# Kernel optimization log

Hardware: AMD Instinct MI355X
Metric: run time of the kernel (lower is better)

The kernel has to match this reference:

```python
import jax, jax.numpy as jnp
import numpy as np

D_MODEL = 1024
NUM_HEADS = 16
D_K = D_MODEL // NUM_HEADS
B, S = 2, 2048


def setup_inputs() -> dict:
    key = jax.random.key(0)
    ks = jax.random.split(key, 11)
    sc = 1.0 / np.sqrt(D_MODEL)
    return {
        "Q_input": jax.random.normal(ks[0], (B, S, D_MODEL), jnp.float32),
        "K_input": jax.random.normal(ks[1], (B, S, D_MODEL), jnp.float32),
        "V_input": jax.random.normal(ks[2], (B, S, D_MODEL), jnp.float32),
        "Wq": jax.random.normal(ks[3], (D_MODEL, D_MODEL), jnp.float32) * sc,
        "bq": jax.random.normal(ks[4], (D_MODEL,), jnp.float32) * 0.01,
        "Wk": jax.random.normal(ks[5], (D_MODEL, D_MODEL), jnp.float32) * sc,
        "bk": jax.random.normal(ks[6], (D_MODEL,), jnp.float32) * 0.01,
        "Wv": jax.random.normal(ks[7], (D_MODEL, D_MODEL), jnp.float32) * sc,
        "bv": jax.random.normal(ks[8], (D_MODEL,), jnp.float32) * 0.01,
        "Wo": jax.random.normal(ks[9], (D_MODEL, D_MODEL), jnp.float32) * sc,
        "bo": jax.random.normal(ks[10], (D_MODEL,), jnp.float32) * 0.01,
    }


def reference(Q_input, K_input, V_input, Wq, bq, Wk, bk, Wv, bv, Wo, bo):
    # Linear projections (torch Linear: x @ W.T + b)
    Q = Q_input @ Wq.T + bq  # [B,S,D]
    K = K_input @ Wk.T + bk
    V = V_input @ Wv.T + bv
    # split heads -> [B,H,S,dk]
    def split(x):
        return x.reshape(B, S, NUM_HEADS, D_K).transpose(0, 2, 1, 3)
    Qh, Kh, Vh = split(Q), split(K), split(V)
    scale = 1.0 / jnp.sqrt(jnp.asarray(D_K, Qh.dtype))
    scores = jnp.einsum('bhqd,bhkd->bhqk', Qh, Kh) * scale  # [B,H,S,S]
    attn = jax.nn.softmax(scores, axis=-1)
    ctx = jnp.einsum('bhqk,bhkd->bhqd', attn, Vh)  # [B,H,S,dk]
    concat = ctx.transpose(0, 2, 1, 3).reshape(B, S, D_MODEL)
    out = concat @ Wo.T + bo  # dropout is identity in eval
    return out
```

## Files before the change

kernel.cpp:

```cpp
#include <hip/hip_runtime.h>
#include <stdint.h>

#define DM   1024
#define NH   16
#define DKH  64
#define BBATCH 2
#define SEQ  2048
#define MTOK (BBATCH*SEQ)

typedef unsigned short u16;
typedef unsigned int   u32;
typedef __attribute__((ext_vector_type(8))) short  bf16x8;
typedef __attribute__((ext_vector_type(4))) float  f32x4;

struct PtrArr11 { const void* p[11]; };
struct U16Arr11 { u16* p[11]; };

__device__ __forceinline__ float bf2f(u16 u) {
  union { unsigned int i; float f; } z; z.i = ((unsigned int)u) << 16; return z.f;
}
__device__ __forceinline__ u16 f2bf(float f) {
  union { float f; unsigned int i; } z; z.f = f;
  unsigned int i = z.i + 0x7fffu + ((z.i >> 16) & 1u);
  return (u16)(i >> 16);
}

__device__ __forceinline__ bf16x8 u4_to_bf(u32 a, u32 b, u32 c, u32 d) {
  union { u32 u[4]; bf16x8 v; } z; z.u[0] = a; z.u[1] = b; z.u[2] = c; z.u[3] = d; return z.v;
}

__device__ __forceinline__ void gld16(const void* g, void* l) {
  __builtin_amdgcn_global_load_lds(
      (const __attribute__((address_space(1))) void*)g,
      (__attribute__((address_space(3))) void*)l,
      16, 0, 0);
}

__global__ void k_detect(const unsigned int* __restrict__ w, int* __restrict__ flag) {
  const int ln = threadIdx.x & 63;
  const unsigned int word = w[ln];
  const unsigned int ex = (word >> 7) & 0xFFu;
  const int hit = (ex >= 100u && ex <= 126u) ? 1 : 0;
  unsigned long long m = __ballot(hit);
  if (ln == 0) *flag = (__popcll(m) >= 40) ? 0 : 1;
}

__global__ __launch_bounds__(256) void k_convert_all(PtrArr11 src, U16Arr11 dst,
                                                     const int* __restrict__ flag) {
  if (*flag == 0) return;
  const int b = blockIdx.x;
  int seg, base;
  if      (b <  2048) { seg = 0;  base = 0;    }
  else if (b <  4096) { seg = 1;  base = 2048; }
  else if (b <  6144) { seg = 2;  base = 4096; }
  else if (b <  6656) { seg = 3;  base = 6144; }
  else if (b == 6656) { seg = 4;  base = 6656; }
  else if (b <  7169) { seg = 5;  base = 6657; }
  else if (b == 7169) { seg = 6;  base = 7169; }
  else if (b <  7682) { seg = 7;  base = 7170; }
  else if (b == 7682) { seg = 8;  base = 7682; }
  else if (b <  8195) { seg = 9;  base = 7683; }
  else                { seg = 10; base = 8195; }
  const int n = (seg < 3) ? (MTOK * DM) : ((seg & 1) ? (DM * DM) : DM);
  const int i0 = (b - base) * 2048 + threadIdx.x * 8;
  if (i0 >= n) return;
  const float* s = (const float*)src.p[seg] + i0;
  bf16x8 o;
#pragma unroll
  for (int j = 0; j < 8; ++j) o[j] = (short)f2bf(s[j]);
  *(bf16x8*)(dst.p[seg] + i0) = o;
}

__device__ __forceinline__ void gemm_body(const u16* __restrict__ X,
                                          const u16* __restrict__ W,
                                          const u16* __restrict__ bias,
                                          void* __restrict__ out,
                                          int isf32out)
{
  __shared__ __attribute__((aligned(16))) u16 sA[128 * 32];
  __shared__ __attribute__((aligned(16))) u16 sB[128 * 32];
  const int tid = threadIdx.x;
  const int ln = tid & 63, wv = tid >> 6;
  const int wm = wv & 1, wn = wv >> 1;
  const int m0 = blockIdx.y * 128, n0 = blockIdx.x * 128;
  const int fr = ln & 15, fq = ln >> 4;
  const int srow = ln >> 2, sslot = (ln & 3) * 8;

  f32x4 acc[4][4];
#pragma unroll
  for (int i = 0; i < 4; ++i)
#pragma unroll
    for (int j = 0; j < 4; ++j) acc[i][j] = (f32x4){0.f, 0.f, 0.f, 0.f};

  const u16* pA = X + (size_t)(m0 + wv * 32 + srow) * DM + sslot;
  const u16* pB = W + (size_t)(n0 + wv * 32 + srow) * DM + sslot;
  u16* lA0 = sA + (wv * 2) * 512; u16* lA1 = sA + (wv * 2 + 1) * 512;
  u16* lB0 = sB + (wv * 2) * 512; u16* lB1 = sB + (wv * 2 + 1) * 512;

  for (int k0 = 0; k0 < DM; k0 += 32) {
    gld16(pA + k0,            lA0);
    gld16(pA + 16 * DM + k0,  lA1);
    gld16(pB + k0,            lB0);
    gld16(pB + 16 * DM + k0,  lB1);
    asm volatile("s_waitcnt vmcnt(0)" ::: "memory");
    __syncthreads();

    bf16x8 af[4], bfg[4];
#pragma unroll
    for (int t = 0; t < 4; ++t) {
      af[t]  = *(const bf16x8*)(sA + (wm * 64 + t * 16 + fr) * 32 + fq * 8);
      bfg[t] = *(const bf16x8*)(sB + (wn * 64 + t * 16 + fr) * 32 + fq * 8);
    }
#pragma unroll
    for (int i = 0; i < 4; ++i)
#pragma unroll
      for (int j = 0; j < 4; ++j)
        acc[i][j] = __builtin_amdgcn_mfma_f32_16x16x32_bf16(af[i], bfg[j], acc[i][j], 0, 0, 0);
    __syncthreads();
  }

#pragma unroll
  for (int i = 0; i < 4; ++i) {
    const int row = m0 + wm * 64 + i * 16 + fq * 4;
#pragma unroll
    for (int j = 0; j < 4; ++j) {
      const int col = n0 + wn * 64 + j * 16 + fr;
      const float bv = bf2f(bias[col]);
#pragma unroll
      for (int r = 0; r < 4; ++r) {
        const float val = acc[i][j][r] + bv;
        const size_t idx = (size_t)(row + r) * DM + col;
        if (isf32out) ((float*)out)[idx] = val;
        else          ((u16*)out)[idx]   = f2bf(val);
      }
    }
  }
}

__device__ __forceinline__ void gemm_body_n64(const u16* __restrict__ X,
                                              const u16* __restrict__ W,
                                              const u16* __restrict__ bias,
                                              void* __restrict__ out,
                                              int isf32out)
{
  __shared__ __attribute__((aligned(16))) u16 sA[128 * 32];
  __shared__ __attribute__((aligned(16))) u16 sB[64 * 32];
  const int tid = threadIdx.x;
  const int ln = tid & 63, wv = tid >> 6;
  const int wm = wv >> 1, wn = wv & 1;
  const int m0 = blockIdx.y * 128, n0 = blockIdx.x * 64;
  const int fr = ln & 15, fq = ln >> 4;
  const int srow = ln >> 2, sslot = (ln & 3) * 8;

  f32x4 acc[4][2];
#pragma unroll
  for (int i = 0; i < 4; ++i)
#pragma unroll
    for (int j = 0; j < 2; ++j) acc[i][j] = (f32x4){0.f, 0.f, 0.f, 0.f};

  const u16* pA = X + (size_t)(m0 + wv * 32 + srow) * DM + sslot;
  const u16* pB = W + (size_t)(n0 + wv * 16 + srow) * DM + sslot;
  u16* lA0 = sA + (wv * 2) * 512; u16* lA1 = sA + (wv * 2 + 1) * 512;
  u16* lB  = sB + wv * 512;

  for (int k0 = 0; k0 < DM; k0 += 32) {
    gld16(pA + k0,           lA0);
    gld16(pA + 16 * DM + k0, lA1);
    gld16(pB + k0,           lB);
    asm volatile("s_waitcnt vmcnt(0)" ::: "memory");
    __syncthreads();

    bf16x8 af[4], bfg[2];
#pragma unroll
    for (int t = 0; t < 4; ++t)
      af[t]  = *(const bf16x8*)(sA + (wm * 64 + t * 16 + fr) * 32 + fq * 8);
#pragma unroll
    for (int t = 0; t < 2; ++t)
      bfg[t] = *(const bf16x8*)(sB + (wn * 32 + t * 16 + fr) * 32 + fq * 8);
#pragma unroll
    for (int i = 0; i < 4; ++i)
#pragma unroll
      for (int j = 0; j < 2; ++j)
        acc[i][j] = __builtin_amdgcn_mfma_f32_16x16x32_bf16(af[i], bfg[j], acc[i][j], 0, 0, 0);
    __syncthreads();
  }

#pragma unroll
  for (int i = 0; i < 4; ++i) {
    const int row = m0 + wm * 64 + i * 16 + fq * 4;
#pragma unroll
    for (int j = 0; j < 2; ++j) {
      const int col = n0 + wn * 32 + j * 16 + fr;
      const float bv = bf2f(bias[col]);
#pragma unroll
      for (int r = 0; r < 4; ++r) {
        const float val = acc[i][j][r] + bv;
        const size_t idx = (size_t)(row + r) * DM + col;
        if (isf32out) ((float*)out)[idx] = val;
        else          ((u16*)out)[idx]   = f2bf(val);
      }
    }
  }
}

__global__ __launch_bounds__(256, 2) void k_gemm_qkv(
    PtrArr11 orig, U16Arr11 conv, const int* __restrict__ flag,
    u16* oq, u16* ok, u16* ov)
{
  const int f = *flag;
  const int z = blockIdx.z;
  const u16* X  = f ? conv.p[z]         : (const u16*)orig.p[z];
  const u16* W  = f ? conv.p[3 + 2 * z] : (const u16*)orig.p[3 + 2 * z];
  const u16* bi = f ? conv.p[4 + 2 * z] : (const u16*)orig.p[4 + 2 * z];
  u16* o = (z == 0) ? oq : (z == 1) ? ok : ov;
  gemm_body(X, W, bi, o, 0);
}

__global__ __launch_bounds__(256, 2) void k_gemm_one(
    const u16* X, const void* Wo_o, const u16* Wo_c,
    const void* bo_o, const u16* bo_c, const int* __restrict__ flag, void* o)
{
  const int f = *flag;
  const u16* W  = f ? Wo_c : (const u16*)Wo_o;
  const u16* bi = f ? bo_c : (const u16*)bo_o;
  gemm_body_n64(X, W, bi, o, f);
}

__global__ __launch_bounds__(256) void k_transpose(const u16* __restrict__ in,
                                                   u16* __restrict__ out)
{
  __shared__ u16 t[64][66];
  const int b = blockIdx.z;
  const int s0 = blockIdx.x * 64, d0 = blockIdx.y * 64;
  const int c = threadIdx.x & 63, r0 = threadIdx.x >> 6;
#pragma unroll
  for (int i = 0; i < 16; ++i) {
    const int r = r0 + 4 * i;
    t[r][c] = in[(size_t)(b * SEQ + s0 + r) * DM + d0 + c];
  }
  __syncthreads();
#pragma unroll
  for (int i = 0; i < 16; ++i) {
    const int r = r0 + 4 * i;
    out[(size_t)(b * DM + d0 + r) * SEQ + s0 + c] = t[c][r];
  }
}

__global__ __launch_bounds__(256, 2) void k_attn(
    const u16* __restrict__ Qp, const u16* __restrict__ Kp,
    const u16* __restrict__ Vt, u16* __restrict__ ctx)
{
  __shared__ __attribute__((aligned(16))) u16 sK[2][64 * 64];

  const int tid = threadIdx.x;
  const int ln = tid & 63, wv = tid >> 6;
  const int bh = blockIdx.y;
  const int b = bh >> 4, h = bh & 15;
  const int q0 = blockIdx.x * 128 + wv * 32;
  const int fr = ln & 15, fq = ln >> 4;
  const int fr7 = fr & 7;

  const int srow = ln >> 3;
  const int scol = ((ln & 7) ^ srow) * 8;
  const u16* gK0 = Kp + (size_t)(b * SEQ + wv * 16 + srow) * DM + h * DKH + scol;
  u16* sKb = &sK[0][0];

  const u16* gVb = Vt + (size_t)(b * DM + h * DKH) * SEQ;

  bf16x8 qf[2][2];
#pragma unroll
  for (int qt = 0; qt < 2; ++qt)
#pragma unroll
    for (int ks = 0; ks < 2; ++ks) {
      const u16* src = Qp + (size_t)(b * SEQ + q0 + qt * 16 + fr) * DM + h * DKH + ks * 32 + fq * 8;
      bf16x8 v = *(const bf16x8*)src;
      bf16x8 w;
#pragma unroll
      for (int j = 0; j < 8; ++j) w[j] = (short)f2bf(bf2f((u16)v[j]) * 0.125f);
      qf[qt][ks] = w;
    }

  float l_a[2] = {0.f, 0.f};
  float l_b[2] = {0.f, 0.f};
  f32x4 o_acc[2][4];
#pragma unroll
  for (int qt = 0; qt < 2; ++qt)
#pragma unroll
    for (int dt = 0; dt < 4; ++dt) o_acc[qt][dt] = (f32x4){0.f, 0.f, 0.f, 0.f};

#define STAGE_K(pp, key0)                                      \
  do {                                                         \
    u16* kd = sKb + (pp) * 4096 + wv * 1024;                   \
    gld16(gK0 + (size_t)(key0) * DM, kd);                      \
    gld16(gK0 + (size_t)((key0) + 8) * DM, kd + 512);          \
  } while (0)

  STAGE_K(0, 0);
  asm volatile("s_waitcnt vmcnt(0)" ::: "memory");
  __syncthreads();

  int p = 0;
  for (int kb = 0; kb < SEQ / 64; ++kb) {
    const int key0 = kb * 64;

    bf16x8 vf[4][2];
#pragma unroll
    for (int dt = 0; dt < 4; ++dt)
#pragma unroll
      for (int ks = 0; ks < 2; ++ks)
        vf[dt][ks] = *(const bf16x8*)(gVb + (size_t)(dt * 16 + fr) * SEQ + key0 + ks * 32 + fq * 8);

    if (kb + 1 < SEQ / 64) STAGE_K(p ^ 1, key0 + 64);

    const u16* K = sKb + p * 4096;

    bf16x8 kf[4][2];
#pragma unroll
    for (int nt = 0; nt < 4; ++nt)
#pragma unroll
      for (int ks = 0; ks < 2; ++ks)
        kf[nt][ks] = *(const bf16x8*)(K + (nt * 16 + fr) * 64 + ((ks * 4 + fq) ^ fr7) * 8);

    u32 pw[2][2][4];
#pragma unroll
    for (int qt = 0; qt < 2; ++qt) {
      f32x4 s_acc[4];
#pragma unroll
      for (int nt = 0; nt < 4; ++nt) s_acc[nt] = (f32x4){0.f, 0.f, 0.f, 0.f};
      __builtin_amdgcn_s_setprio(1);
#pragma unroll
      for (int nt = 0; nt < 4; ++nt)
#pragma unroll
        for (int ks = 0; ks < 2; ++ks)
          s_acc[nt] = __builtin_amdgcn_mfma_f32_16x16x32_bf16(kf[nt][ks], qf[qt][ks], s_acc[nt], 0, 0, 0);
      __builtin_amdgcn_s_setprio(0);

      u32 w[4][2];
#pragma unroll
      for (int nt = 0; nt < 4; ++nt)
#pragma unroll
        for (int t = 0; t < 2; ++t) {
          const float e0 = __expf(s_acc[nt][2 * t]);
          const float e1 = __expf(s_acc[nt][2 * t + 1]);
          l_a[qt] += e0;
          l_b[qt] += e1;
          u32 wd;
          asm("v_cvt_pk_bf16_f32 %0, %1, %2" : "=v"(wd) : "v"(e0), "v"(e1));
          w[nt][t] = wd;
        }
#pragma unroll
      for (int ks = 0; ks < 2; ++ks) {
        u32 a0 = w[2 * ks][0], b0 = w[2 * ks + 1][0];
        u32 a1 = w[2 * ks][1], b1 = w[2 * ks + 1][1];
        asm("v_permlane32_swap_b32 %0, %1" : "+v"(a0), "+v"(b0));
        asm("v_permlane16_swap_b32 %0, %1" : "+v"(a0), "+v"(b0));
        asm("v_permlane32_swap_b32 %0, %1" : "+v"(a1), "+v"(b1));
        asm("v_permlane16_swap_b32 %0, %1" : "+v"(a1), "+v"(b1));
        pw[qt][ks][0] = a0; pw[qt][ks][1] = a1; pw[qt][ks][2] = b0; pw[qt][ks][3] = b1;
      }
    }

#pragma unroll
    for (int dt = 0; dt < 4; ++dt) {
      __builtin_amdgcn_s_setprio(1);
#pragma unroll
      for (int qt = 0; qt < 2; ++qt) {
        o_acc[qt][dt] = __builtin_amdgcn_mfma_f32_16x16x32_bf16(
            u4_to_bf(pw[qt][0][0], pw[qt][0][1], pw[qt][0][2], pw[qt][0][3]), vf[dt][0], o_acc[qt][dt], 0, 0, 0);
        o_acc[qt][dt] = __builtin_amdgcn_mfma_f32_16x16x32_bf16(
            u4_to_bf(pw[qt][1][0], pw[qt][1][1], pw[qt][1][2], pw[qt][1][3]), vf[dt][1], o_acc[qt][dt], 0, 0, 0);
      }
      __builtin_amdgcn_s_setprio(0);
    }

    asm volatile("s_waitcnt vmcnt(0)" ::: "memory");
    __syncthreads();
    p ^= 1;
  }
#undef STAGE_K

  float iv[2][4];
#pragma unroll
  for (int qt = 0; qt < 2; ++qt) {
    float t = l_a[qt] + l_b[qt];
    t += __shfl_xor(t, 16);
    t += __shfl_xor(t, 32);
    const float rl = 1.0f / t;
#pragma unroll
    for (int rr = 0; rr < 4; ++rr) iv[qt][rr] = __shfl(rl, fq * 4 + rr);
  }
#pragma unroll
  for (int qt = 0; qt < 2; ++qt)
#pragma unroll
    for (int dt = 0; dt < 4; ++dt)
#pragma unroll
      for (int r = 0; r < 4; ++r) {
        const int qrow = q0 + qt * 16 + fq * 4 + r;
        const int col = h * DKH + dt * 16 + fr;
        ctx[(size_t)(b * SEQ + qrow) * DM + col] = f2bf(o_acc[qt][dt][r] * iv[qt][r]);
      }
}

extern "C" void kernel_launch(void* const* d_in, const int* in_sizes, int n_in,
                              void* d_out, int out_size, void* d_ws, size_t ws_size,
                              hipStream_t stream)
{
  char* ws = (char*)d_ws;
  int* flag = (int*)ws;

  const size_t TOKSZ = (size_t)MTOK * DM * sizeof(u16);
  const size_t WSZ   = (size_t)DM * DM * sizeof(u16);
  const size_t BSZ   = 4096;

  size_t off = 256;
  u16* Qc  = (u16*)(ws + off); off += TOKSZ;
  u16* Kc  = (u16*)(ws + off); off += TOKSZ;
  u16* Vc  = (u16*)(ws + off); off += TOKSZ;
  u16* Wqc = (u16*)(ws + off); off += WSZ;
  u16* Wkc = (u16*)(ws + off); off += WSZ;
  u16* Wvc = (u16*)(ws + off); off += WSZ;
  u16* Woc = (u16*)(ws + off); off += WSZ;
  u16* bqc = (u16*)(ws + off); off += BSZ;
  u16* bkc = (u16*)(ws + off); off += BSZ;
  u16* bvc = (u16*)(ws + off); off += BSZ;
  u16* boc = (u16*)(ws + off); off += BSZ;
  u16* Qp  = (u16*)(ws + off); off += TOKSZ;
  u16* Kp  = (u16*)(ws + off); off += TOKSZ;
  u16* Vp  = (u16*)(ws + off); off += TOKSZ;
  u16* Vt  = Qc;
  u16* ctx = Kc;

  PtrArr11 orig;
  for (int i = 0; i < 11; ++i) orig.p[i] = d_in[i];
  U16Arr11 conv;
  conv.p[0] = Qc;  conv.p[1] = Kc;  conv.p[2] = Vc;
  conv.p[3] = Wqc; conv.p[4] = bqc; conv.p[5] = Wkc; conv.p[6] = bkc;
  conv.p[7] = Wvc; conv.p[8] = bvc; conv.p[9] = Woc; conv.p[10] = boc;

  dim3 blk(256);

  k_detect<<<1, 64, 0, stream>>>((const unsigned int*)d_in[3], flag);
  k_convert_all<<<8196, blk, 0, stream>>>(orig, conv, flag);
  k_gemm_qkv<<<dim3(DM / 128, MTOK / 128, 3), blk, 0, stream>>>(
      orig, conv, flag, Qp, Kp, Vp);
  k_transpose<<<dim3(SEQ / 64, DM / 64, BBATCH), blk, 0, stream>>>(Vp, Vt);
  k_attn<<<dim3(SEQ / 128, BBATCH * NH), blk, 0, stream>>>(Qp, Kp, Vt, ctx);
  k_gemm_one<<<dim3(DM / 64, MTOK / 128, 1), blk, 0, stream>>>(
      ctx, d_in[9], Woc, d_in[10], boc, flag, d_out);
}
```

Measured before the change: 248.4 us.

## Use BK=64 swizzled QKV GEMM, stage V in LDS, vectorize f32 conversion

The QKV projection GEMM now uses a K-tile of 64 with an XOR-swizzled LDS layout, which halves the number of barrier/wait iterations and avoids bank conflicts. The attention kernel now double-buffers V tiles through LDS alongside K, where before each wave read V fragments straight from global memory. The fp32-to-bf16 conversion kernel uses 16-byte vector loads. In exchange, LDS use per block goes up in both the GEMM and the attention kernel, which could reduce occupancy.

```diff
diff --git a/kernel.cpp b/kernel.cpp
--- a/kernel.cpp
+++ b/kernel.cpp
@@ -65,26 +65,32 @@
   const int i0 = (b - base) * 2048 + threadIdx.x * 8;
   if (i0 >= n) return;
   const float* s = (const float*)src.p[seg] + i0;
+  const f32x4 x0 = *(const f32x4*)(s);
+  const f32x4 x1 = *(const f32x4*)(s + 4);
   bf16x8 o;
 #pragma unroll
-  for (int j = 0; j < 8; ++j) o[j] = (short)f2bf(s[j]);
+  for (int j = 0; j < 4; ++j) o[j] = (short)f2bf(x0[j]);
+#pragma unroll
+  for (int j = 0; j < 4; ++j) o[4 + j] = (short)f2bf(x1[j]);
   *(bf16x8*)(dst.p[seg] + i0) = o;
 }
 
-__device__ __forceinline__ void gemm_body(const u16* __restrict__ X,
-                                          const u16* __restrict__ W,
-                                          const u16* __restrict__ bias,
-                                          void* __restrict__ out,
-                                          int isf32out)
-{
-  __shared__ __attribute__((aligned(16))) u16 sA[128 * 32];
-  __shared__ __attribute__((aligned(16))) u16 sB[128 * 32];
+__device__ __forceinline__ void gemm_body64(const u16* __restrict__ X,
+                                            const u16* __restrict__ W,
+                                            const u16* __restrict__ bias,
+                                            void* __restrict__ out,
+                                            int isf32out)
+{
+  __shared__ __attribute__((aligned(16))) u16 sA[128 * 64];
+  __shared__ __attribute__((aligned(16))) u16 sB[128 * 64];
   const int tid = threadIdx.x;
   const int ln = tid & 63, wv = tid >> 6;
   const int wm = wv & 1, wn = wv >> 1;
   const int m0 = blockIdx.y * 128, n0 = blockIdx.x * 128;
   const int fr = ln & 15, fq = ln >> 4;
-  const int srow = ln >> 2, sslot = (ln & 3) * 8;
+  const int fr7 = fr & 7;
+  const int srow = ln >> 3;
+  const int scol = ((ln & 7) ^ srow) * 8;
 
   f32x4 acc[4][4];
 #pragma unroll
@@ -92,30 +98,35 @@
 #pragma unroll
     for (int j = 0; j < 4; ++j) acc[i][j] = (f32x4){0.f, 0.f, 0.f, 0.f};
 
-  const u16* pA = X + (size_t)(m0 + wv * 32 + srow) * DM + sslot;
-  const u16* pB = W + (size_t)(n0 + wv * 32 + srow) * DM + sslot;
-  u16* lA0 = sA + (wv * 2) * 512; u16* lA1 = sA + (wv * 2 + 1) * 512;
-  u16* lB0 = sB + (wv * 2) * 512; u16* lB1 = sB + (wv * 2 + 1) * 512;
-
-  for (int k0 = 0; k0 < DM; k0 += 32) {
-    gld16(pA + k0,            lA0);
-    gld16(pA + 16 * DM + k0,  lA1);
-    gld16(pB + k0,            lB0);
-    gld16(pB + 16 * DM + k0,  lB1);
+  const u16* pA = X + (size_t)(m0 + wv * 32 + srow) * DM + scol;
+  const u16* pB = W + (size_t)(n0 + wv * 32 + srow) * DM + scol;
+  u16* lA = sA + wv * 32 * 64;
+  u16* lB = sB + wv * 32 * 64;
+
+  for (int k0 = 0; k0 < DM; k0 += 64) {
+#pragma unroll
+    for (int c = 0; c < 4; ++c) {
+      gld16(pA + (size_t)(c * 8) * DM + k0, lA + c * 8 * 64);
+      gld16(pB + (size_t)(c * 8) * DM + k0, lB + c * 8 * 64);
+    }
     asm volatile("s_waitcnt vmcnt(0)" ::: "memory");
     __syncthreads();
 
-    bf16x8 af[4], bfg[4];
-#pragma unroll
-    for (int t = 0; t < 4; ++t) {
-      af[t]  = *(const bf16x8*)(sA + (wm * 64 + t * 16 + fr) * 32 + fq * 8);
-      bfg[t] = *(const bf16x8*)(sB + (wn * 64 + t * 16 + fr) * 32 + fq * 8);
-    }
+    bf16x8 af[4][2], bfg[4][2];
+#pragma unroll
+    for (int t = 0; t < 4; ++t)
+#pragma unroll
+      for (int ks = 0; ks < 2; ++ks) {
+        af[t][ks]  = *(const bf16x8*)(sA + (wm * 64 + t * 16 + fr) * 64 + ((ks * 4 + fq) ^ fr7) * 8);
+        bfg[t][ks] = *(const bf16x8*)(sB + (wn * 64 + t * 16 + fr) * 64 + ((ks * 4 + fq) ^ fr7) * 8);
+      }
 #pragma unroll
     for (int i = 0; i < 4; ++i)
 #pragma unroll
-      for (int j = 0; j < 4; ++j)
-        acc[i][j] = __builtin_amdgcn_mfma_f32_16x16x32_bf16(af[i], bfg[j], acc[i][j], 0, 0, 0);
+      for (int j = 0; j < 4; ++j) {
+        acc[i][j] = __builtin_amdgcn_mfma_f32_16x16x32_bf16(af[i][0], bfg[j][0], acc[i][j], 0, 0, 0);
+        acc[i][j] = __builtin_amdgcn_mfma_f32_16x16x32_bf16(af[i][1], bfg[j][1], acc[i][j], 0, 0, 0);
+      }
     __syncthreads();
   }
 
@@ -213,7 +224,7 @@
   const u16* W  = f ? conv.p[3 + 2 * z] : (const u16*)orig.p[3 + 2 * z];
   const u16* bi = f ? conv.p[4 + 2 * z] : (const u16*)orig.p[4 + 2 * z];
   u16* o = (z == 0) ? oq : (z == 1) ? ok : ov;
-  gemm_body(X, W, bi, o, 0);
+  gemm_body64(X, W, bi, o, 0);
 }
 
 __global__ __launch_bounds__(256, 2) void k_gemm_one(
@@ -251,6 +262,7 @@
     const u16* __restrict__ Vt, u16* __restrict__ ctx)
 {
   __shared__ __attribute__((aligned(16))) u16 sK[2][64 * 64];
+  __shared__ __attribute__((aligned(16))) u16 sV[2][64 * 64];
 
   const int tid = threadIdx.x;
   const int ln = tid & 63, wv = tid >> 6;
@@ -263,9 +275,9 @@
   const int srow = ln >> 3;
   const int scol = ((ln & 7) ^ srow) * 8;
   const u16* gK0 = Kp + (size_t)(b * SEQ + wv * 16 + srow) * DM + h * DKH + scol;
+  const u16* gV0 = Vt + (size_t)(b * DM + h * DKH + wv * 16 + srow) * SEQ + scol;
   u16* sKb = &sK[0][0];
-
-  const u16* gVb = Vt + (size_t)(b * DM + h * DKH) * SEQ;
+  u16* sVb = &sV[0][0];
 
   bf16x8 qf[2][2];
 #pragma unroll
@@ -288,31 +300,26 @@
 #pragma unroll
     for (int dt = 0; dt < 4; ++dt) o_acc[qt][dt] = (f32x4){0.f, 0.f, 0.f, 0.f};
 
-#define STAGE_K(pp, key0)                                      \
+#define STAGE_KV(pp, key0)                                     \
   do {                                                         \
     u16* kd = sKb + (pp) * 4096 + wv * 1024;                   \
+    u16* vd = sVb + (pp) * 4096 + wv * 1024;                   \
     gld16(gK0 + (size_t)(key0) * DM, kd);                      \
     gld16(gK0 + (size_t)((key0) + 8) * DM, kd + 512);          \
+    gld16(gV0 + (key0), vd);                                   \
+    gld16(gV0 + (key0) + 8 * SEQ, vd + 512);                   \
   } while (0)
 
-  STAGE_K(0, 0);
+  STAGE_KV(0, 0);
   asm volatile("s_waitcnt vmcnt(0)" ::: "memory");
   __syncthreads();
 
   int p = 0;
   for (int kb = 0; kb < SEQ / 64; ++kb) {
-    const int key0 = kb * 64;
-
-    bf16x8 vf[4][2];
-#pragma unroll
-    for (int dt = 0; dt < 4; ++dt)
-#pragma unroll
-      for (int ks = 0; ks < 2; ++ks)
-        vf[dt][ks] = *(const bf16x8*)(gVb + (size_t)(dt * 16 + fr) * SEQ + key0 + ks * 32 + fq * 8);
-
-    if (kb + 1 < SEQ / 64) STAGE_K(p ^ 1, key0 + 64);
+    if (kb + 1 < SEQ / 64) STAGE_KV(p ^ 1, (kb + 1) * 64);
 
     const u16* K = sKb + p * 4096;
+    const u16* V = sVb + p * 4096;
 
     bf16x8 kf[4][2];
 #pragma unroll
@@ -362,13 +369,15 @@
 
 #pragma unroll
     for (int dt = 0; dt < 4; ++dt) {
+      bf16x8 vf0 = *(const bf16x8*)(V + (dt * 16 + fr) * 64 + ((0 + fq) ^ fr7) * 8);
+      bf16x8 vf1 = *(const bf16x8*)(V + (dt * 16 + fr) * 64 + ((4 + fq) ^ fr7) * 8);
       __builtin_amdgcn_s_setprio(1);
 #pragma unroll
       for (int qt = 0; qt < 2; ++qt) {
         o_acc[qt][dt] = __builtin_amdgcn_mfma_f32_16x16x32_bf16(
-            u4_to_bf(pw[qt][0][0], pw[qt][0][1], pw[qt][0][2], pw[qt][0][3]), vf[dt][0], o_acc[qt][dt], 0, 0, 0);
+            u4_to_bf(pw[qt][0][0], pw[qt][0][1], pw[qt][0][2], pw[qt][0][3]), vf0, o_acc[qt][dt], 0, 0, 0);
         o_acc[qt][dt] = __builtin_amdgcn_mfma_f32_16x16x32_bf16(
-            u4_to_bf(pw[qt][1][0], pw[qt][1][1], pw[qt][1][2], pw[qt][1][3]), vf[dt][1], o_acc[qt][dt], 0, 0, 0);
+            u4_to_bf(pw[qt][1][0], pw[qt][1][1], pw[qt][1][2], pw[qt][1][3]), vf1, o_acc[qt][dt], 0, 0, 0);
       }
       __builtin_amdgcn_s_setprio(0);
     }
@@ -377,7 +386,7 @@
     __syncthreads();
     p ^= 1;
   }
-#undef STAGE_K
+#undef STAGE_KV
 
   float iv[2][4];
 #pragma unroll
```

New measurement: 235.5 us. 5.2% less time.
